# Kernel tuning notes

Measured on AMD Instinct MI355X. Metric: run time of the kernel, lower is better.

## Reference

```python
import jax, jax.numpy as jnp
import numpy as np

# Architecture constants (from module defaults)
D, H, DH, P, G, DEPTH, M, NCLS = 192, 3, 64, 16, 14, 12, 128, 1000  # M = feature_map_dim // 2
EXITS = (4, 8, 12)
TEMP = 1.0 / np.sqrt(DH)  # Favor softmax_temp = 1/sqrt(d_head)
EPS_ATTN = 1e-6           # fast_transformers LinearAttention eps
LN_EPS = 1e-5


def ln(x, g, b):
    mu = x.mean(-1, keepdims=True)
    var = ((x - mu) ** 2).mean(-1, keepdims=True)
    return (x - mu) * jax.lax.rsqrt(var + LN_EPS) * g + b


def favor(x, omega):
    # FAVOR+ positive random features for the softmax kernel.
    # x: [B,L,H,DH], omega: [DH,M] -> phi: [B,L,H,2M]
    xs = x * np.float32(np.sqrt(TEMP))
    off = 0.5 * (xs * xs).sum(-1, keepdims=True)
    u = jnp.einsum('blhd,dm->blhm', xs, omega)
    phi = jnp.concatenate([jnp.exp(u - off), jnp.exp(-u - off)], axis=-1)
    return phi * np.float32(1.0 / np.sqrt(2 * M))


def forward(x, patch_w, patch_b, pe_ln_g, pe_ln_b, cls_token, pos_embed,
            Wq, bq, Wk, bk, Wv, bv, Wo, bo,
            ln1_g, ln1_b, ln2_g, ln2_b, lnb_g, lnb_b,
            W1, b1, W2, b2, omega, head_w, head_b):
    B = x.shape[0]
    # Patch embedding: Conv2d(k=16, s=16) == blocked einsum
    xp = x.reshape(B, 3, G, P, G, P)
    tok = jnp.einsum('bchpwq,dcpq->bhwd', xp, patch_w).reshape(B, G * G, D) + patch_b
    tok = ln(tok, pe_ln_g, pe_ln_b)  # PatchEmbed.norm (norm_layer=LayerNorm)
    tok = jnp.concatenate([jnp.broadcast_to(cls_token, (B, 1, D)), tok], axis=1) + pos_embed
    xc = tok  # [B, 197, D]
    outs = []
    for i in range(DEPTH):
        # --- linear (FAVOR) attention ---
        q = (xc @ Wq[i].T + bq[i]).reshape(B, -1, H, DH)
        k = (xc @ Wk[i].T + bk[i]).reshape(B, -1, H, DH)
        v = (xc @ Wv[i].T + bv[i]).reshape(B, -1, H, DH)
        Qp = favor(q, omega[i])
        Kp = favor(k, omega[i])
        KV = jnp.einsum('bshm,bshd->bhmd', Kp, v)
        Z = 1.0 / (jnp.einsum('blhm,bhm->blh', Qp, Kp.sum(axis=1)) + EPS_ATTN)
        attn = jnp.einsum('blhm,bhmd,blh->blhd', Qp, KV, Z).reshape(B, -1, D)
        # fast_transformers TransformerEncoderLayer (post-norm style)
        xc = xc + attn @ Wo[i].T + bo[i]
        y = xc = ln(xc, ln1_g[i], ln1_b[i])
        y = jax.nn.relu(y @ W1[i].T + b1[i]) @ W2[i].T + b2[i]
        xc = ln(xc + y, ln2_g[i], ln2_b[i])
        # per-block TransformerEncoder final norm (builder final_normalization)
        xc = ln(xc, lnb_g[i], lnb_b[i])
        if (i + 1) in EXITS:
            j = EXITS.index(i + 1)
            z = xc.mean(axis=1)  # AdaptiveAvgPool1d(1) over sequence
            outs.append(z @ head_w[j].T + head_b[j])
    return tuple(outs)


def setup_inputs() -> dict:
    key = jax.random.key(0)
    ks = iter(jax.random.split(key, 32))
    n = lambda shape, s=0.02: jax.random.normal(next(ks), shape, jnp.float32) * s
    return dict(
        x=jax.random.normal(next(ks), (64, 3, 224, 224), jnp.float32),
        patch_w=n((D, 3, P, P)), patch_b=jnp.zeros((D,), jnp.float32),
        pe_ln_g=jnp.ones((D,), jnp.float32), pe_ln_b=jnp.zeros((D,), jnp.float32),
        cls_token=n((1, 1, D)), pos_embed=n((1, G * G + 1, D)),
        Wq=n((DEPTH, D, D)), bq=jnp.zeros((DEPTH, D), jnp.float32),
        Wk=n((DEPTH, D, D)), bk=jnp.zeros((DEPTH, D), jnp.float32),
        Wv=n((DEPTH, D, D)), bv=jnp.zeros((DEPTH, D), jnp.float32),
        Wo=n((DEPTH, D, D)), bo=jnp.zeros((DEPTH, D), jnp.float32),
        ln1_g=jnp.ones((DEPTH, D), jnp.float32), ln1_b=jnp.zeros((DEPTH, D), jnp.float32),
        ln2_g=jnp.ones((DEPTH, D), jnp.float32), ln2_b=jnp.zeros((DEPTH, D), jnp.float32),
        lnb_g=jnp.ones((DEPTH, D), jnp.float32), lnb_b=jnp.zeros((DEPTH, D), jnp.float32),
        W1=n((DEPTH, 4 * D, D)), b1=jnp.zeros((DEPTH, 4 * D), jnp.float32),
        W2=n((DEPTH, D, 4 * D)), b2=jnp.zeros((DEPTH, D), jnp.float32),
        omega=jax.random.normal(next(ks), (DEPTH, DH, M), jnp.float32),
        head_w=n((len(EXITS), NCLS, D)), head_b=jnp.zeros((len(EXITS), NCLS), jnp.float32),
    )


def reference(x, patch_w, patch_b, pe_ln_g, pe_ln_b, cls_token, pos_embed,
              Wq, bq, Wk, bk, Wv, bv, Wo, bo,
              ln1_g, ln1_b, ln2_g, ln2_b, lnb_g, lnb_b,
              W1, b1, W2, b2, omega, head_w, head_b):
    return forward(x, patch_w, patch_b, pe_ln_g, pe_ln_b, cls_token, pos_embed,
                   Wq, bq, Wk, bk, Wv, bv, Wo, bo,
                   ln1_g, ln1_b, ln2_g, ln2_b, lnb_g, lnb_b,
                   W1, b1, W2, b2, omega, head_w, head_b)
```

## Files before the change

### kernel.cpp

```cpp
#include <hip/hip_runtime.h>
#include <math.h>

#define BB     64
#define LLEN   197
#define BLROWS 12608
#define MPAD   12672
#define DMODEL 192
#define NHEAD  3
#define DHEAD  64
#define M2FEAT 256
#define FFDIM  768
#define NDEPTH 12
#define NCLS   1000
#define NPATCH 196
#define BPROWS 12544
#define KPATCH 768
#define PHIRS  264
#define PHTRS  40
#define VLT    208

#define MODE_PLAIN 0
#define MODE_RELU  1
#define MODE_QKV   2

typedef unsigned short ushort;
typedef __attribute__((ext_vector_type(8))) short bf16x8;
typedef __attribute__((ext_vector_type(4))) float floatx4;
typedef __attribute__((ext_vector_type(4))) short short4v;

__device__ __forceinline__ float wave_reduce_sum(float v) {
#pragma unroll
  for (int s = 32; s > 0; s >>= 1) v += __shfl_xor(v, s, 64);
  return v;
}
__device__ __forceinline__ ushort f2bf(float f) {
  unsigned u = __float_as_uint(f);
  return (ushort)((u + 0x7fffu + ((u >> 16) & 1u)) >> 16);
}
__device__ __forceinline__ float bf2f(ushort u) {
  return __uint_as_float(((unsigned)u) << 16);
}
__device__ __forceinline__ void gll16(const ushort* g, ushort* l) {
  __builtin_amdgcn_global_load_lds(
      (const __attribute__((address_space(1))) void*)g,
      (__attribute__((address_space(3))) void*)l, 16, 0, 0);
}

__global__ void zero_buf(uint4* __restrict__ p, int n16) {
  const int i = blockIdx.x * 256 + threadIdx.x;
  if (i < n16) p[i] = uint4{0, 0, 0, 0};
}

__global__ __launch_bounds__(256) void gemm_128(
    const ushort* __restrict__ A, int lda,
    const ushort* __restrict__ W, int ldw,
    const float* __restrict__ bias,
    ushort* __restrict__ C, int ldc, ushort* __restrict__ Vt,
    int Ndim, int Kdim, int mode)
{
  __shared__ __align__(16) ushort As[2][128 * 64];
  __shared__ __align__(16) ushort Ws[2][128 * 64];
  const int tid = threadIdx.x;
  const int bm = blockIdx.x, bn = blockIdx.y;
  const int wave = tid >> 6, lane = tid & 63;
  const int wm = (wave >> 1) * 64, wn = (wave & 1) * 64;
  const int quad = lane >> 4, l16 = lane & 15;
  const int srow = lane >> 3;
  const int scol = ((lane & 7) ^ srow) * 8;
  const ushort* Ap = A + (size_t)(bm * 128) * lda;
  const ushort* Wp = W + (size_t)(bn * 128) * ldw;
  floatx4 acc[4][4] = {};
  const int nT = Kdim >> 6;
#pragma unroll
  for (int t = 0; t < 4; ++t) {
    const int rb = (t * 4 + wave) * 8;
    gll16(Ap + (size_t)(rb + srow) * lda + scol, &As[0][rb * 64]);
    gll16(Wp + (size_t)(rb + srow) * ldw + scol, &Ws[0][rb * 64]);
  }
  for (int kt = 0; kt < nT; ++kt) {
    const int cur = kt & 1;
    __syncthreads();
    if (kt + 1 < nT) {
      const int kk = (kt + 1) * 64, nxt = cur ^ 1;
#pragma unroll
      for (int t = 0; t < 4; ++t) {
        const int rb = (t * 4 + wave) * 8;
        gll16(Ap + (size_t)(rb + srow) * lda + kk + scol, &As[nxt][rb * 64]);
        gll16(Wp + (size_t)(rb + srow) * ldw + kk + scol, &Ws[nxt][rb * 64]);
      }
    }
#pragma unroll
    for (int ks = 0; ks < 2; ++ks) {
      bf16x8 af[4], bf[4];
#pragma unroll
      for (int i = 0; i < 4; ++i) {
        const int ra = wm + i * 16 + l16, rw = wn + i * 16 + l16;
        af[i] = *(const bf16x8*)&As[cur][ra * 64 + ((((ks << 2) | quad) ^ (ra & 7)) * 8)];
        bf[i] = *(const bf16x8*)&Ws[cur][rw * 64 + ((((ks << 2) | quad) ^ (rw & 7)) * 8)];
      }
#pragma unroll
      for (int i = 0; i < 4; ++i)
#pragma unroll
        for (int j = 0; j < 4; ++j)
          acc[i][j] = __builtin_amdgcn_mfma_f32_16x16x32_bf16(af[i], bf[j], acc[i][j], 0, 0, 0);
    }
  }
  if (mode == MODE_QKV) {
#pragma unroll
    for (int i = 0; i < 4; ++i)
#pragma unroll
      for (int r = 0; r < 4; ++r) {
        const int grow = bm * 128 + wm + i * 16 + quad * 4 + r;
        const int bidx = grow / 197;
        const int lloc = grow - bidx * 197;
#pragma unroll
        for (int j = 0; j < 4; ++j) {
          const int col = bn * 128 + wn + j * 16 + l16;
          if (col >= Ndim) continue;
          const float o = acc[i][j][r] + bias[col];
          if (col < 384) {
            C[(size_t)grow * ldc + col] = f2bf(o);
          } else if (grow < BLROWS) {
            const int h = (col - 384) >> 6, d = (col - 384) & 63;
            Vt[((size_t)(bidx * 3 + h) * 64 + d) * VLT + lloc] = f2bf(o);
          }
        }
      }
  } else {
#pragma unroll
    for (int j = 0; j < 4; ++j) {
      const int col = bn * 128 + wn + j * 16 + l16;
      if (col >= Ndim) continue;
      const float bv = bias[col];
#pragma unroll
      for (int i = 0; i < 4; ++i)
#pragma unroll
        for (int r = 0; r < 4; ++r) {
          const int grow = bm * 128 + wm + i * 16 + quad * 4 + r;
          float o = acc[i][j][r] + bv;
          if (mode == MODE_RELU) o = fmaxf(o, 0.f);
          C[(size_t)grow * ldc + col] = f2bf(o);
        }
    }
  }
}

__global__ __launch_bounds__(256) void gemm_bf2(
    const ushort* __restrict__ A, int lda,
    const ushort* __restrict__ W, int ldw,
    const float* __restrict__ bias,
    ushort* __restrict__ C, int ldc, int Kdim, int mode)
{
  __shared__ __align__(16) ushort As[2][128 * 64];
  __shared__ __align__(16) ushort Ws[2][64 * 64];
  const int tid = threadIdx.x;
  const int bm = blockIdx.x, bn = blockIdx.y;
  const int wave = tid >> 6, lane = tid & 63;
  const int wm = (wave >> 1) * 64, wn = (wave & 1) * 32;
  const int quad = lane >> 4, l16 = lane & 15;
  const int srow = lane >> 3;
  const int scol = ((lane & 7) ^ srow) * 8;
  const ushort* Ap = A + (size_t)(bm * 128) * lda;
  const ushort* Wp = W + (size_t)(bn * 64) * ldw;
  floatx4 acc[4][2] = {};
  const int nT = Kdim >> 6;
#pragma unroll
  for (int t = 0; t < 4; ++t) {
    const int rb = (t * 4 + wave) * 8;
    gll16(Ap + (size_t)(rb + srow) * lda + scol, &As[0][rb * 64]);
  }
#pragma unroll
  for (int t = 0; t < 2; ++t) {
    const int rb = (t * 4 + wave) * 8;
    gll16(Wp + (size_t)(rb + srow) * ldw + scol, &Ws[0][rb * 64]);
  }
  for (int kt = 0; kt < nT; ++kt) {
    const int cur = kt & 1;
    __syncthreads();
    if (kt + 1 < nT) {
      const int kk = (kt + 1) * 64, nxt = cur ^ 1;
#pragma unroll
      for (int t = 0; t < 4; ++t) {
        const int rb = (t * 4 + wave) * 8;
        gll16(Ap + (size_t)(rb + srow) * lda + kk + scol, &As[nxt][rb * 64]);
      }
#pragma unroll
      for (int t = 0; t < 2; ++t) {
        const int rb = (t * 4 + wave) * 8;
        gll16(Wp + (size_t)(rb + srow) * ldw + kk + scol, &Ws[nxt][rb * 64]);
      }
    }
#pragma unroll
    for (int ks = 0; ks < 2; ++ks) {
      bf16x8 af[4], bf[2];
#pragma unroll
      for (int i = 0; i < 4; ++i) {
        const int ra = wm + i * 16 + l16;
        af[i] = *(const bf16x8*)&As[cur][ra * 64 + ((((ks << 2) | quad) ^ (ra & 7)) * 8)];
      }
#pragma unroll
      for (int j = 0; j < 2; ++j) {
        const int rw = wn + j * 16 + l16;
        bf[j] = *(const bf16x8*)&Ws[cur][rw * 64 + ((((ks << 2) | quad) ^ (rw & 7)) * 8)];
      }
#pragma unroll
      for (int i = 0; i < 4; ++i)
#pragma unroll
        for (int j = 0; j < 2; ++j)
          acc[i][j] = __builtin_amdgcn_mfma_f32_16x16x32_bf16(af[i], bf[j], acc[i][j], 0, 0, 0);
    }
  }
#pragma unroll
  for (int j = 0; j < 2; ++j) {
    const int col = bn * 64 + wn + j * 16 + l16;
    const float bv = bias[col];
#pragma unroll
    for (int i = 0; i < 4; ++i)
#pragma unroll
      for (int r = 0; r < 4; ++r) {
        const int grow = bm * 128 + wm + i * 16 + quad * 4 + r;
        float o = acc[i][j][r] + bv;
        if (mode == MODE_RELU) o = fmaxf(o, 0.f);
        C[(size_t)grow * ldc + col] = f2bf(o);
      }
  }
}

__global__ __launch_bounds__(256) void gemm_ln(
    const ushort* __restrict__ A, int lda,
    const ushort* __restrict__ W, int ldw,
    const float* __restrict__ bias,
    ushort* __restrict__ XC,
    const float* __restrict__ ga, const float* __restrict__ ba,
    const float* __restrict__ gb, const float* __restrict__ bb,
    int Kdim, int dln)
{
  __shared__ __align__(16) ushort As[2][64 * 64];
  __shared__ __align__(16) ushort Ws[2][192 * 64];
  const int tid = threadIdx.x;
  const int bm = blockIdx.x;
  const int wave = tid >> 6, lane = tid & 63;
  const int quad = lane >> 4, l16 = lane & 15;
  const int srow = lane >> 3;
  const int scol = ((lane & 7) ^ srow) * 8;
  const ushort* Ap = A + (size_t)(bm * 64) * lda;
  floatx4 acc[12] = {};
  const int nT = Kdim >> 6;
#pragma unroll
  for (int t = 0; t < 2; ++t) {
    const int rb = (t * 4 + wave) * 8;
    gll16(Ap + (size_t)(rb + srow) * lda + scol, &As[0][rb * 64]);
  }
#pragma unroll
  for (int t = 0; t < 6; ++t) {
    const int rb = (t * 4 + wave) * 8;
    gll16(W + (size_t)(rb + srow) * ldw + scol, &Ws[0][rb * 64]);
  }
  for (int kt = 0; kt < nT; ++kt) {
    const int cur = kt & 1;
    __syncthreads();
    if (kt + 1 < nT) {
      const int kk = (kt + 1) * 64, nxt = cur ^ 1;
#pragma unroll
      for (int t = 0; t < 2; ++t) {
        const int rb = (t * 4 + wave) * 8;
        gll16(Ap + (size_t)(rb + srow) * lda + kk + scol, &As[nxt][rb * 64]);
      }
#pragma unroll
      for (int t = 0; t < 6; ++t) {
        const int rb = (t * 4 + wave) * 8;
        gll16(W + (size_t)(rb + srow) * ldw + kk + scol, &Ws[nxt][rb * 64]);
      }
    }
#pragma unroll
    for (int ks = 0; ks < 2; ++ks) {
      const int ra = wave * 16 + l16;
      const bf16x8 af = *(const bf16x8*)&As[cur][ra * 64 + ((((ks << 2) | quad) ^ (ra & 7)) * 8)];
#pragma unroll
      for (int j = 0; j < 12; ++j) {
        const int rw = j * 16 + l16;
        const bf16x8 bf = *(const bf16x8*)&Ws[cur][rw * 64 + ((((ks << 2) | quad) ^ (rw & 7)) * 8)];
        acc[j] = __builtin_amdgcn_mfma_f32_16x16x32_bf16(af, bf, acc[j], 0, 0, 0);
      }
    }
  }
#pragma unroll
  for (int r = 0; r < 4; ++r) {
    const int row = bm * 64 + wave * 16 + quad * 4 + r;
    ushort* xp = XC + (size_t)row * DMODEL;
    float xr[12];
    float s = 0.f, sq = 0.f;
#pragma unroll
    for (int j = 0; j < 12; ++j) {
      const int col = j * 16 + l16;
      const float o = acc[j][r] + bias[col] + bf2f(xp[col]);
      xr[j] = o; s += o; sq += o * o;
    }
#pragma unroll
    for (int m = 1; m < 16; m <<= 1) {
      s += __shfl_xor(s, m, 64); sq += __shfl_xor(sq, m, 64);
    }
    float mu = s * (1.f / 192.f);
    float var = sq * (1.f / 192.f) - mu * mu;
    float rs = rsqrtf(var + 1e-5f);
#pragma unroll
    for (int j = 0; j < 12; ++j) {
      const int col = j * 16 + l16;
      xr[j] = (xr[j] - mu) * rs * ga[col] + ba[col];
    }
    if (dln) {
      float s2 = 0.f, sq2 = 0.f;
#pragma unroll
      for (int j = 0; j < 12; ++j) { s2 += xr[j]; sq2 += xr[j] * xr[j]; }
#pragma unroll
      for (int m = 1; m < 16; m <<= 1) {
        s2 += __shfl_xor(s2, m, 64); sq2 += __shfl_xor(sq2, m, 64);
      }
      mu = s2 * (1.f / 192.f);
      var = sq2 * (1.f / 192.f) - mu * mu;
      rs = rsqrtf(var + 1e-5f);
#pragma unroll
      for (int j = 0; j < 12; ++j) {
        const int col = j * 16 + l16;
        xr[j] = (xr[j] - mu) * rs * gb[col] + bb[col];
      }
    }
#pragma unroll
    for (int j = 0; j < 12; ++j) xp[j * 16 + l16] = f2bf(xr[j]);
  }
}

__global__ __launch_bounds__(256) void kv_fused(
    const ushort* __restrict__ qkv, const ushort* __restrict__ OmT,
    const ushort* __restrict__ Vt, ushort* __restrict__ KVt)
{
  __shared__ __align__(16) ushort Ks[32 * 64];
  __shared__ __align__(16) ushort Om[64 * 64];
  __shared__ __align__(16) ushort PhT[128 * PHTRS];
  __shared__ __align__(16) ushort Vts[2][64 * 32];
  __shared__ __align__(16) ushort Vcst[16 * 32];
  __shared__ float offs[32];
  const int tid = threadIdx.x;
  const int bh = blockIdx.x, mh = blockIdx.y;
  const int b = bh / 3, h = bh - b * 3;
  const int wave = tid >> 6, lane = tid & 63;
  const int quad = lane >> 4, l16 = lane & 15;
  const int lr8 = lane >> 3, g8 = lane & 7;
  const int lr4 = lane >> 2, g4 = lane & 3;
#pragma unroll
  for (int t = 0; t < 2; ++t) {
    const int rb = (t * 4 + wave) * 8;
    const int row = rb + lr8;
    gll16(OmT + (size_t)(mh * 64 + row) * 64 + ((g8 ^ (row & 7)) * 8), &Om[rb * 64]);
  }
  {
    const int rowK = wave * 8 + lr8;
    gll16(qkv + (size_t)(b * 197 + rowK) * 576 + 192 + h * 64 + ((g8 ^ (rowK & 7)) * 8),
          &Ks[wave * 8 * 64]);
    const int rowV = wave * 16 + lr4;
    gll16(Vt + ((size_t)bh * 64 + rowV) * VLT + ((g4 ^ (rowV & 3)) * 8),
          &Vts[0][wave * 16 * 32]);
  }
  for (int e = tid; e < 16 * 32; e += 256) Vcst[e] = (e < 32) ? 0x3F80 : 0;
  floatx4 acc[2][5] = {};
  for (int c = 0; c < 7; ++c) {
    const int l0 = c * 32;
    const int cur = c & 1;
    __syncthreads();
    if (tid < 64) {
      const int row = tid >> 1, half = tid & 1;
      float s = 0.f;
#pragma unroll
      for (int t = 0; t < 4; ++t) {
        bf16x8 v8 = *(const bf16x8*)&Ks[row * 64 + (((half * 4 + t) ^ (row & 7)) * 8)];
#pragma unroll
        for (int q = 0; q < 8; ++q) { float xv = bf2f((ushort)v8[q]); s += xv * xv; }
      }
      s += __shfl_xor(s, 1, 64);
      if (half == 0) offs[row] = 0.0625f * s;
    }
    floatx4 ui[2] = {};
#pragma unroll
    for (int ksb = 0; ksb < 2; ++ksb) {
      bf16x8 af[2], bfm;
#pragma unroll
      for (int i = 0; i < 2; ++i) {
        const int row = i * 16 + l16;
        af[i] = *(const bf16x8*)&Ks[row * 64 + (((quad + (ksb << 2)) ^ (row & 7)) * 8)];
      }
      {
        const int row = wave * 16 + l16;
        bfm = *(const bf16x8*)&Om[row * 64 + (((quad + (ksb << 2)) ^ (row & 7)) * 8)];
      }
#pragma unroll
      for (int i = 0; i < 2; ++i)
        ui[i] = __builtin_amdgcn_mfma_f32_16x16x32_bf16(af[i], bfm, ui[i], 0, 0, 0);
    }
    __syncthreads();
    {
      const int mloc = wave * 16 + l16;
#pragma unroll
      for (int i = 0; i < 2; ++i) {
#pragma unroll
        for (int r = 0; r < 4; ++r) {
          const int ll = i * 16 + quad * 4 + r;
          float ep = 0.f, em = 0.f;
          if (l0 + ll < 197) {
            const float off = offs[ll];
            const float u = ui[i][r];
            ep = __expf(u - off) * 0.0625f;
            em = __expf(-u - off) * 0.0625f;
          }
          PhT[mloc * PHTRS + ll] = f2bf(ep);
          PhT[(64 + mloc) * PHTRS + ll] = f2bf(em);
        }
      }
    }
    if (c + 1 < 7) {
      const int rowK = wave * 8 + lr8;
      const int lK = (c + 1) * 32 + rowK;
      gll16(qkv + (size_t)(b * 197 + lK) * 576 + 192 + h * 64 + ((g8 ^ (rowK & 7)) * 8),
            &Ks[wave * 8 * 64]);
      const int rowV = wave * 16 + lr4;
      gll16(Vt + ((size_t)bh * 64 + rowV) * VLT + (c + 1) * 32 + ((g4 ^ (rowV & 3)) * 8),
            &Vts[cur ^ 1][wave * 16 * 32]);
    }
    __syncthreads();
    bf16x8 af[2], bf[5];
#pragma unroll
    for (int i = 0; i < 2; ++i)
      af[i] = *(const bf16x8*)&PhT[(wave * 32 + i * 16 + l16) * PHTRS + quad * 8];
#pragma unroll
    for (int j = 0; j < 4; ++j) {
      const int row = j * 16 + l16;
      bf[j] = *(const bf16x8*)&Vts[cur][row * 32 + ((quad ^ (row & 3)) * 8)];
    }
    bf[4] = *(const bf16x8*)&Vcst[l16 * 32 + quad * 8];
#pragma unroll
    for (int i = 0; i < 2; ++i)
#pragma unroll
      for (int j = 0; j < 5; ++j)
        acc[i][j] = __builtin_amdgcn_mfma_f32_16x16x32_bf16(af[i], bf[j], acc[i][j], 0, 0, 0);
  }
#pragma unroll
  for (int i = 0; i < 2; ++i) {
    const int prow0 = wave * 32 + i * 16 + quad * 4;
    const int f0 = (prow0 < 64) ? (mh * 64 + prow0) : (128 + mh * 64 + prow0 - 64);
#pragma unroll
    for (int j = 0; j < 5; ++j) {
      const int d = j * 16 + l16;
      short4v pk;
#pragma unroll
      for (int r = 0; r < 4; ++r) pk[r] = (short)f2bf(acc[i][j][r]);
      *(short4v*)(KVt + ((size_t)bh * 80 + d) * 256 + f0) = pk;
    }
  }
}

__global__ __launch_bounds__(256) void attn_fused(
    const ushort* __restrict__ qkv, const ushort* __restrict__ OmT,
    const ushort* __restrict__ KVt, ushort* __restrict__ OUT)
{
  __shared__ __align__(16) ushort Phi[64 * PHIRS];
  __shared__ __align__(16) ushort Bs[2][80 * 32];
  __shared__ float offs[64];
  __shared__ float zs[64];
  ushort* Qs = Phi;
  ushort* Om = Phi + 64 * 64;
  const int tid = threadIdx.x;
  const int bx = blockIdx.x, bh = blockIdx.y;
  const int b = bh / 3, h = bh - b * 3;
  const int wave = tid >> 6, lane = tid & 63;
  const int quad = lane >> 4, l16 = lane & 15;
  const int lr8 = lane >> 3, g8 = lane & 7;
  const int lr4 = lane >> 2, g4 = lane & 3;
#pragma unroll
  for (int t = 0; t < 2; ++t) {
    const int rb = wave * 16 + t * 8;
    const int row = rb + lr8;
    const int l = bx * 64 + row;
    gll16(qkv + (size_t)(b * 197 + l) * 576 + h * 64 + ((g8 ^ (row & 7)) * 8), &Qs[rb * 64]);
  }
#pragma unroll
  for (int t = 0; t < 4; ++t) {
    const int rb = wave * 32 + t * 8;
    const int row = rb + lr8;
    gll16(OmT + (size_t)row * 64 + ((g8 ^ (row & 7)) * 8), &Om[rb * 64]);
  }
  __syncthreads();
  if (tid < 128) {
    const int row = tid >> 1, half = tid & 1;
    float s = 0.f;
#pragma unroll
    for (int t = 0; t < 4; ++t) {
      bf16x8 v8 = *(const bf16x8*)&Qs[row * 64 + (((half * 4 + t) ^ (row & 7)) * 8)];
#pragma unroll
      for (int q = 0; q < 8; ++q) { float xv = bf2f((ushort)v8[q]); s += xv * xv; }
    }
    s += __shfl_xor(s, 1, 64);
    if (half == 0) offs[row] = 0.0625f * s;
  }
  floatx4 uacc[8] = {};
#pragma unroll
  for (int ksb = 0; ksb < 2; ++ksb) {
    bf16x8 af, bf[8];
    {
      const int row = wave * 16 + l16;
      af = *(const bf16x8*)&Qs[row * 64 + (((quad + (ksb << 2)) ^ (row & 7)) * 8)];
    }
#pragma unroll
    for (int j = 0; j < 8; ++j) {
      const int row = j * 16 + l16;
      bf[j] = *(const bf16x8*)&Om[row * 64 + (((quad + (ksb << 2)) ^ (row & 7)) * 8)];
    }
#pragma unroll
    for (int j = 0; j < 8; ++j)
      uacc[j] = __builtin_amdgcn_mfma_f32_16x16x32_bf16(af, bf[j], uacc[j], 0, 0, 0);
  }
  __syncthreads();
#pragma unroll
  for (int r = 0; r < 4; ++r) {
    const int l = wave * 16 + quad * 4 + r;
    const float off = offs[l];
#pragma unroll
    for (int j = 0; j < 8; ++j) {
      const int m = j * 16 + l16;
      const float u = uacc[j][r];
      Phi[l * PHIRS + m]       = f2bf(__expf(u - off)  * 0.0625f);
      Phi[l * PHIRS + m + 128] = f2bf(__expf(-u - off) * 0.0625f);
    }
  }
  const ushort* Bp = KVt + (size_t)bh * 80 * 256;
  {
    const int row = wave * 16 + lr4;
    gll16(Bp + (size_t)row * 256 + ((g4 ^ (row & 3)) * 8), &Bs[0][wave * 16 * 32]);
    if (wave == 0)
      gll16(Bp + (size_t)(64 + lr4) * 256 + ((g4 ^ (lr4 & 3)) * 8), &Bs[0][64 * 32]);
  }
  floatx4 acc[5] = {};
  for (int c = 0; c < 8; ++c) {
    const int cur = c & 1;
    __syncthreads();
    if (c + 1 < 8) {
      const int m0 = (c + 1) * 32, nxt = cur ^ 1;
      const int row = wave * 16 + lr4;
      gll16(Bp + (size_t)row * 256 + m0 + ((g4 ^ (row & 3)) * 8), &Bs[nxt][wave * 16 * 32]);
      if (wave == 0)
        gll16(Bp + (size_t)(64 + lr4) * 256 + m0 + ((g4 ^ (lr4 & 3)) * 8), &Bs[nxt][64 * 32]);
    }
    const int m0 = c * 32;
    bf16x8 af, bf[5];
    af = *(const bf16x8*)&Phi[(wave * 16 + l16) * PHIRS + m0 + quad * 8];
#pragma unroll
    for (int j = 0; j < 5; ++j) {
      const int row = j * 16 + l16;
      bf[j] = *(const bf16x8*)&Bs[cur][row * 32 + ((quad ^ (row & 3)) * 8)];
    }
#pragma unroll
    for (int j = 0; j < 5; ++j)
      acc[j] = __builtin_amdgcn_mfma_f32_16x16x32_bf16(af, bf[j], acc[j], 0, 0, 0);
  }
  if (l16 == 0) {
#pragma unroll
    for (int r = 0; r < 4; ++r)
      zs[wave * 16 + quad * 4 + r] = acc[4][r];
  }
  __syncthreads();
#pragma unroll
  for (int r = 0; r < 4; ++r) {
    const int ll = wave * 16 + quad * 4 + r;
    const int l = bx * 64 + ll;
    if (l >= 197) continue;
    const float z = 1.f / (zs[ll] + 1e-6f);
#pragma unroll
    for (int j = 0; j < 4; ++j)
      OUT[(size_t)(b * 197 + l) * 192 + h * 64 + j * 16 + l16] =
          f2bf(acc[j][r] * z);
  }
}

__global__ void conv_qkv(const float* __restrict__ Wq, const float* __restrict__ Wk,
                         const float* __restrict__ Wv, const float* __restrict__ bq,
                         const float* __restrict__ bk, const float* __restrict__ bv,
                         ushort* __restrict__ dst, float* __restrict__ bdst) {
  const int l = blockIdx.y;
  const int e = blockIdx.x * 256 + threadIdx.x;
  const int n = e / 192, k = e - n * 192;
  const float* src;
  if (n < 192)      src = Wq + (size_t)l * 36864 + n * 192;
  else if (n < 384) src = Wk + (size_t)l * 36864 + (n - 192) * 192;
  else              src = Wv + (size_t)l * 36864 + (n - 384) * 192;
  dst[(size_t)l * 640 * 192 + e] = f2bf(src[k]);
  if (e < 576) {
    float bvv;
    if (e < 192)      bvv = bq[l * 192 + e];
    else if (e < 384) bvv = bk[l * 192 + e - 192];
    else              bvv = bv[l * 192 + e - 384];
    bdst[l * 576 + e] = bvv;
  }
}

__global__ void conv_pad(const float* __restrict__ src, ushort* __restrict__ dst,
                         int NK, int padNK) {
  const int l = blockIdx.y;
  const int e = blockIdx.x * 256 + threadIdx.x;
  if (e < NK) dst[(size_t)l * padNK + e] = f2bf(src[(size_t)l * NK + e]);
}

__global__ void conv_omt(const float* __restrict__ om, ushort* __restrict__ dst) {
  const int l = blockIdx.y;
  const int e = blockIdx.x * 256 + threadIdx.x;
  const int m = e >> 6, d = e & 63;
  dst[(size_t)l * 8192 + e] = f2bf(0.35355339059327379f * om[(size_t)l * 8192 + d * 128 + m]);
}

__global__ __launch_bounds__(256) void im2col_kernel(
    const float* __restrict__ X, ushort* __restrict__ Apd)
{
  const int bp = blockIdx.x;
  const int b = bp / NPATCH, p = bp - b * NPATCH;
  const int gh = p / 14, gw = p - gh * 14;
  for (int e = threadIdx.x; e < KPATCH; e += 256) {
    const int c = e >> 8, rem = e & 255, ph = rem >> 4, pw = rem & 15;
    Apd[(size_t)bp * KPATCH + e] =
        f2bf(X[((size_t)(b * 3 + c) * 224 + gh * 16 + ph) * 224 + gw * 16 + pw]);
  }
}

__global__ __launch_bounds__(256) void assemble_kernel(
    const ushort* __restrict__ TK, const float* __restrict__ g,
    const float* __restrict__ bt, const float* __restrict__ cls,
    const float* __restrict__ pos, ushort* __restrict__ XC)
{
  const int w = threadIdx.x >> 6, lane = threadIdx.x & 63;
  const int row = blockIdx.x * 4 + w;
  const int b = row / LLEN, l = row - b * LLEN;
  float o0, o1, o2;
  if (l == 0) {
    o0 = cls[lane]; o1 = cls[lane + 64]; o2 = cls[lane + 128];
  } else {
    const ushort* tp = TK + (size_t)(b * NPATCH + l - 1) * DMODEL;
    const float x0 = bf2f(tp[lane]), x1 = bf2f(tp[lane + 64]), x2 = bf2f(tp[lane + 128]);
    const float s  = wave_reduce_sum(x0 + x1 + x2);
    const float sq = wave_reduce_sum(x0 * x0 + x1 * x1 + x2 * x2);
    const float mu = s * (1.f / 192.f);
    const float var = sq * (1.f / 192.f) - mu * mu;
    const float rs = rsqrtf(var + 1e-5f);
    o0 = (x0 - mu) * rs * g[lane]       + bt[lane];
    o1 = (x1 - mu) * rs * g[lane + 64]  + bt[lane + 64];
    o2 = (x2 - mu) * rs * g[lane + 128] + bt[lane + 128];
  }
  o0 += pos[l * DMODEL + lane];
  o1 += pos[l * DMODEL + lane + 64];
  o2 += pos[l * DMODEL + lane + 128];
  ushort* xp = XC + (size_t)row * DMODEL;
  xp[lane] = f2bf(o0); xp[lane + 64] = f2bf(o1); xp[lane + 128] = f2bf(o2);
}

__global__ __launch_bounds__(256) void head_kernel(
    const ushort* __restrict__ XC, const float* __restrict__ HW,
    const float* __restrict__ HB, float* __restrict__ OUTp)
{
  __shared__ float zsh[DMODEL];
  const int b = blockIdx.y;
  const int tid = threadIdx.x;
  const int wave = tid >> 6, lane = tid & 63;
  if (wave < 3) {
    const int d = wave * 64 + lane;
    const ushort* xp = XC + (size_t)b * LLEN * DMODEL + d;
    float s = 0.f;
#pragma unroll 4
    for (int l = 0; l < LLEN; ++l) s += bf2f(xp[(size_t)l * DMODEL]);
    zsh[d] = s * (1.f / 197.f);
  }
  __syncthreads();
  const int n = blockIdx.x * 256 + tid;
  if (n < NCLS) {
    const float* w = HW + (size_t)n * DMODEL;
    float s = HB[n];
#pragma unroll 4
    for (int d = 0; d < DMODEL; ++d) s = fmaf(zsh[d], w[d], s);
    OUTp[(size_t)b * NCLS + n] = s;
  }
}

extern "C" void kernel_launch(void* const* d_in, const int* in_sizes, int n_in,
                              void* d_out, int out_size, void* d_ws, size_t ws_size,
                              hipStream_t stream) {
  const float* x        = (const float*)d_in[0];
  const float* patch_w  = (const float*)d_in[1];
  const float* patch_b  = (const float*)d_in[2];
  const float* pe_ln_g  = (const float*)d_in[3];
  const float* pe_ln_b  = (const float*)d_in[4];
  const float* cls_tok  = (const float*)d_in[5];
  const float* pos_emb  = (const float*)d_in[6];
  const float* Wq = (const float*)d_in[7];
  const float* bq = (const float*)d_in[8];
  const float* Wk = (const float*)d_in[9];
  const float* bk = (const float*)d_in[10];
  const float* Wv = (const float*)d_in[11];
  const float* bv = (const float*)d_in[12];
  const float* Wo = (const float*)d_in[13];
  const float* bo = (const float*)d_in[14];
  const float* ln1_g = (const float*)d_in[15];
  const float* ln1_b = (const float*)d_in[16];
  const float* ln2_g = (const float*)d_in[17];
  const float* ln2_b = (const float*)d_in[18];
  const float* lnb_g = (const float*)d_in[19];
  const float* lnb_b = (const float*)d_in[20];
  const float* W1 = (const float*)d_in[21];
  const float* b1 = (const float*)d_in[22];
  const float* W2 = (const float*)d_in[23];
  const float* b2 = (const float*)d_in[24];
  const float* omega  = (const float*)d_in[25];
  const float* head_w = (const float*)d_in[26];
  const float* head_b = (const float*)d_in[27];
  float* out = (float*)d_out;
  char* wsb = (char*)d_ws;

  size_t off = 0;
  auto carve = [&](size_t bytes) { size_t o = off; off += (bytes + 255) & ~(size_t)255; return o; };
  ushort* xc     = (ushort*)(wsb + carve((size_t)MPAD * 192 * 2));
  ushort* qkv    = (ushort*)(wsb + carve((size_t)MPAD * 576 * 2));
  ushort* ab     = (ushort*)(wsb + carve((size_t)MPAD * 192 * 2));
  ushort* hidden = (ushort*)(wsb + carve((size_t)MPAD * 768 * 2));
  ushort* KVt    = (ushort*)(wsb + carve((size_t)192 * 80 * 256 * 2));
  ushort* Vt     = (ushort*)(wsb + carve((size_t)192 * 64 * VLT * 2 + 1024));
  float*  bqkv   = (float*)(wsb + carve((size_t)12 * 576 * 4));
  ushort* Wqkv_bf = (ushort*)(wsb + carve((size_t)12 * 640 * 192 * 2));
  ushort* Wo_bf   = (ushort*)(wsb + carve((size_t)12 * 256 * 192 * 2));
  ushort* W1_bf   = (ushort*)(wsb + carve((size_t)12 * 768 * 192 * 2));
  ushort* W2_bf   = (ushort*)(wsb + carve((size_t)12 * 256 * 768 * 2));
  ushort* Wp_bf   = (ushort*)(wsb + carve((size_t)256 * 768 * 2));
  ushort* Om_bf   = (ushort*)(wsb + carve((size_t)12 * 128 * 64 * 2));
  ushort* i2c     = hidden;

  {
    const int n16 = (int)(((size_t)192 * 64 * VLT * 2 + 1024) / 16);
    zero_buf<<<(n16 + 255) / 256, 256, 0, stream>>>((uint4*)Vt, n16);
  }

  conv_qkv<<<dim3(432, 12), 256, 0, stream>>>(Wq, Wk, Wv, bq, bk, bv, Wqkv_bf, bqkv);
  conv_pad<<<dim3(144, 12), 256, 0, stream>>>(Wo, Wo_bf, 36864, 256 * 192);
  conv_pad<<<dim3(576, 12), 256, 0, stream>>>(W1, W1_bf, 147456, 768 * 192);
  conv_pad<<<dim3(576, 12), 256, 0, stream>>>(W2, W2_bf, 147456, 256 * 768);
  conv_pad<<<dim3(576, 1), 256, 0, stream>>>(patch_w, Wp_bf, 147456, 256 * 768);
  conv_omt<<<dim3(32, 12), 256, 0, stream>>>(omega, Om_bf);

  im2col_kernel<<<BPROWS, 256, 0, stream>>>(x, i2c);
  gemm_bf2<<<dim3(98, 3), 256, 0, stream>>>(i2c, KPATCH, Wp_bf, KPATCH,
      patch_b, ab, DMODEL, KPATCH, MODE_PLAIN);
  assemble_kernel<<<BLROWS / 4, 256, 0, stream>>>(ab, pe_ln_g, pe_ln_b,
                                                  cls_tok, pos_emb, xc);

  const int exits[3] = {3, 7, 11};
  for (int i = 0; i < NDEPTH; ++i) {
    gemm_128<<<dim3(99, 5), 256, 0, stream>>>(xc, DMODEL,
        Wqkv_bf + (size_t)i * 640 * 192, DMODEL, bqkv + i * 576,
        qkv, 576, Vt, 576, DMODEL, MODE_QKV);
    kv_fused<<<dim3(192, 2), 256, 0, stream>>>(qkv,
        Om_bf + (size_t)i * 8192, Vt, KVt);
    attn_fused<<<dim3(4, 192), 256, 0, stream>>>(qkv,
        Om_bf + (size_t)i * 8192, KVt, ab);
    gemm_ln<<<MPAD / 64, 256, 0, stream>>>(ab, DMODEL,
        Wo_bf + (size_t)i * 256 * 192, DMODEL, bo + i * DMODEL, xc,
        ln1_g + i * DMODEL, ln1_b + i * DMODEL, nullptr, nullptr,
        DMODEL, 0);
    gemm_128<<<dim3(99, 6), 256, 0, stream>>>(xc, DMODEL,
        W1_bf + (size_t)i * 768 * 192, DMODEL, b1 + i * FFDIM,
        hidden, FFDIM, nullptr, FFDIM, DMODEL, MODE_RELU);
    gemm_ln<<<MPAD / 64, 256, 0, stream>>>(hidden, FFDIM,
        W2_bf + (size_t)i * 256 * 768, FFDIM, b2 + i * DMODEL, xc,
        ln2_g + i * DMODEL, ln2_b + i * DMODEL,
        lnb_g + i * DMODEL, lnb_b + i * DMODEL,
        FFDIM, 1);

    for (int j = 0; j < 3; ++j) {
      if (i == exits[j]) {
        head_kernel<<<dim3(4, BB), 256, 0, stream>>>(
            xc, head_w + (size_t)j * NCLS * DMODEL, head_b + (size_t)j * NCLS,
            out + (size_t)j * BB * NCLS);
      }
    }
  }
}
```

Measured before the change: 1.491 ms.

## Shrink GEMM tiles and split LN-fused GEMM rows across waves

Drops the 128x128 GEMM kernel and routes the QKV and FFN1 projections through the 128x64-tile kernel, which gains the QKV epilogue that scatters V transposed. The LayerNorm-fused output GEMM moves from 64-row to 32-row blocks, with each row's 192 columns split across two waves and row statistics combined through shared memory. The aim is more blocks per launch and better CU fill on these small-N problems. In exchange it reloads more A data, adds barriers and shared-memory reductions, and wastes the padded QKV column tile less.

After: 1.322 ms. -11.3%, faster.

```diff
diff --git a/kernel.cpp b/kernel.cpp
--- a/kernel.cpp
+++ b/kernel.cpp
@@ -51,105 +51,12 @@
   if (i < n16) p[i] = uint4{0, 0, 0, 0};
 }
 
-__global__ __launch_bounds__(256) void gemm_128(
+__global__ __launch_bounds__(256) void gemm_bf2(
     const ushort* __restrict__ A, int lda,
     const ushort* __restrict__ W, int ldw,
     const float* __restrict__ bias,
     ushort* __restrict__ C, int ldc, ushort* __restrict__ Vt,
-    int Ndim, int Kdim, int mode)
-{
-  __shared__ __align__(16) ushort As[2][128 * 64];
-  __shared__ __align__(16) ushort Ws[2][128 * 64];
-  const int tid = threadIdx.x;
-  const int bm = blockIdx.x, bn = blockIdx.y;
-  const int wave = tid >> 6, lane = tid & 63;
-  const int wm = (wave >> 1) * 64, wn = (wave & 1) * 64;
-  const int quad = lane >> 4, l16 = lane & 15;
-  const int srow = lane >> 3;
-  const int scol = ((lane & 7) ^ srow) * 8;
-  const ushort* Ap = A + (size_t)(bm * 128) * lda;
-  const ushort* Wp = W + (size_t)(bn * 128) * ldw;
-  floatx4 acc[4][4] = {};
-  const int nT = Kdim >> 6;
-#pragma unroll
-  for (int t = 0; t < 4; ++t) {
-    const int rb = (t * 4 + wave) * 8;
-    gll16(Ap + (size_t)(rb + srow) * lda + scol, &As[0][rb * 64]);
-    gll16(Wp + (size_t)(rb + srow) * ldw + scol, &Ws[0][rb * 64]);
-  }
-  for (int kt = 0; kt < nT; ++kt) {
-    const int cur = kt & 1;
-    __syncthreads();
-    if (kt + 1 < nT) {
-      const int kk = (kt + 1) * 64, nxt = cur ^ 1;
-#pragma unroll
-      for (int t = 0; t < 4; ++t) {
-        const int rb = (t * 4 + wave) * 8;
-        gll16(Ap + (size_t)(rb + srow) * lda + kk + scol, &As[nxt][rb * 64]);
-        gll16(Wp + (size_t)(rb + srow) * ldw + kk + scol, &Ws[nxt][rb * 64]);
-      }
-    }
-#pragma unroll
-    for (int ks = 0; ks < 2; ++ks) {
-      bf16x8 af[4], bf[4];
-#pragma unroll
-      for (int i = 0; i < 4; ++i) {
-        const int ra = wm + i * 16 + l16, rw = wn + i * 16 + l16;
-        af[i] = *(const bf16x8*)&As[cur][ra * 64 + ((((ks << 2) | quad) ^ (ra & 7)) * 8)];
-        bf[i] = *(const bf16x8*)&Ws[cur][rw * 64 + ((((ks << 2) | quad) ^ (rw & 7)) * 8)];
-      }
-#pragma unroll
-      for (int i = 0; i < 4; ++i)
-#pragma unroll
-        for (int j = 0; j < 4; ++j)
-          acc[i][j] = __builtin_amdgcn_mfma_f32_16x16x32_bf16(af[i], bf[j], acc[i][j], 0, 0, 0);
-    }
-  }
-  if (mode == MODE_QKV) {
-#pragma unroll
-    for (int i = 0; i < 4; ++i)
-#pragma unroll
-      for (int r = 0; r < 4; ++r) {
-        const int grow = bm * 128 + wm + i * 16 + quad * 4 + r;
-        const int bidx = grow / 197;
-        const int lloc = grow - bidx * 197;
-#pragma unroll
-        for (int j = 0; j < 4; ++j) {
-          const int col = bn * 128 + wn + j * 16 + l16;
-          if (col >= Ndim) continue;
-          const float o = acc[i][j][r] + bias[col];
-          if (col < 384) {
-            C[(size_t)grow * ldc + col] = f2bf(o);
-          } else if (grow < BLROWS) {
-            const int h = (col - 384) >> 6, d = (col - 384) & 63;
-            Vt[((size_t)(bidx * 3 + h) * 64 + d) * VLT + lloc] = f2bf(o);
-          }
-        }
-      }
-  } else {
-#pragma unroll
-    for (int j = 0; j < 4; ++j) {
-      const int col = bn * 128 + wn + j * 16 + l16;
-      if (col >= Ndim) continue;
-      const float bv = bias[col];
-#pragma unroll
-      for (int i = 0; i < 4; ++i)
-#pragma unroll
-        for (int r = 0; r < 4; ++r) {
-          const int grow = bm * 128 + wm + i * 16 + quad * 4 + r;
-          float o = acc[i][j][r] + bv;
-          if (mode == MODE_RELU) o = fmaxf(o, 0.f);
-          C[(size_t)grow * ldc + col] = f2bf(o);
-        }
-    }
-  }
-}
-
-__global__ __launch_bounds__(256) void gemm_bf2(
-    const ushort* __restrict__ A, int lda,
-    const ushort* __restrict__ W, int ldw,
-    const float* __restrict__ bias,
-    ushort* __restrict__ C, int ldc, int Kdim, int mode)
+    int Kdim, int mode)
 {
   __shared__ __align__(16) ushort As[2][128 * 64];
   __shared__ __align__(16) ushort Ws[2][64 * 64];
@@ -210,19 +117,41 @@
           acc[i][j] = __builtin_amdgcn_mfma_f32_16x16x32_bf16(af[i], bf[j], acc[i][j], 0, 0, 0);
     }
   }
-#pragma unroll
-  for (int j = 0; j < 2; ++j) {
-    const int col = bn * 64 + wn + j * 16 + l16;
-    const float bv = bias[col];
+  if (mode == MODE_QKV) {
 #pragma unroll
     for (int i = 0; i < 4; ++i)
 #pragma unroll
       for (int r = 0; r < 4; ++r) {
         const int grow = bm * 128 + wm + i * 16 + quad * 4 + r;
-        float o = acc[i][j][r] + bv;
-        if (mode == MODE_RELU) o = fmaxf(o, 0.f);
-        C[(size_t)grow * ldc + col] = f2bf(o);
-      }
+        const int bidx = grow / 197;
+        const int lloc = grow - bidx * 197;
+#pragma unroll
+        for (int j = 0; j < 2; ++j) {
+          const int col = bn * 64 + wn + j * 16 + l16;
+          const float o = acc[i][j][r] + bias[col];
+          if (col < 384) {
+            C[(size_t)grow * ldc + col] = f2bf(o);
+          } else if (grow < BLROWS) {
+            const int h = (col - 384) >> 6, d = (col - 384) & 63;
+            Vt[((size_t)(bidx * 3 + h) * 64 + d) * VLT + lloc] = f2bf(o);
+          }
+        }
+      }
+  } else {
+#pragma unroll
+    for (int j = 0; j < 2; ++j) {
+      const int col = bn * 64 + wn + j * 16 + l16;
+      const float bv = bias[col];
+#pragma unroll
+      for (int i = 0; i < 4; ++i)
+#pragma unroll
+        for (int r = 0; r < 4; ++r) {
+          const int grow = bm * 128 + wm + i * 16 + quad * 4 + r;
+          float o = acc[i][j][r] + bv;
+          if (mode == MODE_RELU) o = fmaxf(o, 0.f);
+          C[(size_t)grow * ldc + col] = f2bf(o);
+        }
+    }
   }
 }
 
@@ -235,22 +164,20 @@
     const float* __restrict__ gb, const float* __restrict__ bb,
     int Kdim, int dln)
 {
-  __shared__ __align__(16) ushort As[2][64 * 64];
+  __shared__ __align__(16) ushort As[2][32 * 64];
   __shared__ __align__(16) ushort Ws[2][192 * 64];
+  __shared__ float p1s[2][32], p1q[2][32], p2s[2][32], p2q[2][32];
   const int tid = threadIdx.x;
   const int bm = blockIdx.x;
   const int wave = tid >> 6, lane = tid & 63;
+  const int rg = wave >> 1, cg = wave & 1;
   const int quad = lane >> 4, l16 = lane & 15;
   const int srow = lane >> 3;
   const int scol = ((lane & 7) ^ srow) * 8;
-  const ushort* Ap = A + (size_t)(bm * 64) * lda;
-  floatx4 acc[12] = {};
+  const ushort* Ap = A + (size_t)(bm * 32) * lda;
+  floatx4 acc[6] = {};
   const int nT = Kdim >> 6;
-#pragma unroll
-  for (int t = 0; t < 2; ++t) {
-    const int rb = (t * 4 + wave) * 8;
-    gll16(Ap + (size_t)(rb + srow) * lda + scol, &As[0][rb * 64]);
-  }
+  gll16(Ap + (size_t)(wave * 8 + srow) * lda + scol, &As[0][wave * 8 * 64]);
 #pragma unroll
   for (int t = 0; t < 6; ++t) {
     const int rb = (t * 4 + wave) * 8;
@@ -261,11 +188,7 @@
     __syncthreads();
     if (kt + 1 < nT) {
       const int kk = (kt + 1) * 64, nxt = cur ^ 1;
-#pragma unroll
-      for (int t = 0; t < 2; ++t) {
-        const int rb = (t * 4 + wave) * 8;
-        gll16(Ap + (size_t)(rb + srow) * lda + kk + scol, &As[nxt][rb * 64]);
-      }
+      gll16(Ap + (size_t)(wave * 8 + srow) * lda + kk + scol, &As[nxt][wave * 8 * 64]);
 #pragma unroll
       for (int t = 0; t < 6; ++t) {
         const int rb = (t * 4 + wave) * 8;
@@ -274,59 +197,85 @@
     }
 #pragma unroll
     for (int ks = 0; ks < 2; ++ks) {
-      const int ra = wave * 16 + l16;
+      const int ra = rg * 16 + l16;
       const bf16x8 af = *(const bf16x8*)&As[cur][ra * 64 + ((((ks << 2) | quad) ^ (ra & 7)) * 8)];
 #pragma unroll
-      for (int j = 0; j < 12; ++j) {
-        const int rw = j * 16 + l16;
+      for (int j = 0; j < 6; ++j) {
+        const int rw = (cg * 6 + j) * 16 + l16;
         const bf16x8 bf = *(const bf16x8*)&Ws[cur][rw * 64 + ((((ks << 2) | quad) ^ (rw & 7)) * 8)];
         acc[j] = __builtin_amdgcn_mfma_f32_16x16x32_bf16(af, bf, acc[j], 0, 0, 0);
       }
     }
   }
+  float xr[4][6];
 #pragma unroll
   for (int r = 0; r < 4; ++r) {
-    const int row = bm * 64 + wave * 16 + quad * 4 + r;
-    ushort* xp = XC + (size_t)row * DMODEL;
-    float xr[12];
+    const int rloc = rg * 16 + quad * 4 + r;
+    const int row = bm * 32 + rloc;
+    const ushort* xp = XC + (size_t)row * DMODEL;
     float s = 0.f, sq = 0.f;
 #pragma unroll
-    for (int j = 0; j < 12; ++j) {
-      const int col = j * 16 + l16;
+    for (int j = 0; j < 6; ++j) {
+      const int col = (cg * 6 + j) * 16 + l16;
       const float o = acc[j][r] + bias[col] + bf2f(xp[col]);
-      xr[j] = o; s += o; sq += o * o;
+      xr[r][j] = o; s += o; sq += o * o;
     }
 #pragma unroll
     for (int m = 1; m < 16; m <<= 1) {
       s += __shfl_xor(s, m, 64); sq += __shfl_xor(sq, m, 64);
     }
-    float mu = s * (1.f / 192.f);
-    float var = sq * (1.f / 192.f) - mu * mu;
-    float rs = rsqrtf(var + 1e-5f);
-#pragma unroll
-    for (int j = 0; j < 12; ++j) {
-      const int col = j * 16 + l16;
-      xr[j] = (xr[j] - mu) * rs * ga[col] + ba[col];
-    }
-    if (dln) {
-      float s2 = 0.f, sq2 = 0.f;
-#pragma unroll
-      for (int j = 0; j < 12; ++j) { s2 += xr[j]; sq2 += xr[j] * xr[j]; }
+    if (l16 == 0) { p1s[cg][rloc] = s; p1q[cg][rloc] = sq; }
+  }
+  __syncthreads();
+#pragma unroll
+  for (int r = 0; r < 4; ++r) {
+    const int rloc = rg * 16 + quad * 4 + r;
+    const float s = p1s[0][rloc] + p1s[1][rloc];
+    const float sq = p1q[0][rloc] + p1q[1][rloc];
+    const float mu = s * (1.f / 192.f);
+    const float var = sq * (1.f / 192.f) - mu * mu;
+    const float rs = rsqrtf(var + 1e-5f);
+#pragma unroll
+    for (int j = 0; j < 6; ++j) {
+      const int col = (cg * 6 + j) * 16 + l16;
+      xr[r][j] = (xr[r][j] - mu) * rs * ga[col] + ba[col];
+    }
+  }
+  if (dln) {
+#pragma unroll
+    for (int r = 0; r < 4; ++r) {
+      const int rloc = rg * 16 + quad * 4 + r;
+      float s = 0.f, sq = 0.f;
+#pragma unroll
+      for (int j = 0; j < 6; ++j) { s += xr[r][j]; sq += xr[r][j] * xr[r][j]; }
 #pragma unroll
       for (int m = 1; m < 16; m <<= 1) {
-        s2 += __shfl_xor(s2, m, 64); sq2 += __shfl_xor(sq2, m, 64);
-      }
-      mu = s2 * (1.f / 192.f);
-      var = sq2 * (1.f / 192.f) - mu * mu;
-      rs = rsqrtf(var + 1e-5f);
-#pragma unroll
-      for (int j = 0; j < 12; ++j) {
-        const int col = j * 16 + l16;
-        xr[j] = (xr[j] - mu) * rs * gb[col] + bb[col];
-      }
-    }
-#pragma unroll
-    for (int j = 0; j < 12; ++j) xp[j * 16 + l16] = f2bf(xr[j]);
+        s += __shfl_xor(s, m, 64); sq += __shfl_xor(sq, m, 64);
+      }
+      if (l16 == 0) { p2s[cg][rloc] = s; p2q[cg][rloc] = sq; }
+    }
+    __syncthreads();
+#pragma unroll
+    for (int r = 0; r < 4; ++r) {
+      const int rloc = rg * 16 + quad * 4 + r;
+      const float s = p2s[0][rloc] + p2s[1][rloc];
+      const float sq = p2q[0][rloc] + p2q[1][rloc];
+      const float mu = s * (1.f / 192.f);
+      const float var = sq * (1.f / 192.f) - mu * mu;
+      const float rs = rsqrtf(var + 1e-5f);
+#pragma unroll
+      for (int j = 0; j < 6; ++j) {
+        const int col = (cg * 6 + j) * 16 + l16;
+        xr[r][j] = (xr[r][j] - mu) * rs * gb[col] + bb[col];
+      }
+    }
+  }
+#pragma unroll
+  for (int r = 0; r < 4; ++r) {
+    const int row = bm * 32 + rg * 16 + quad * 4 + r;
+    ushort* xp = XC + (size_t)row * DMODEL;
+#pragma unroll
+    for (int j = 0; j < 6; ++j) xp[(cg * 6 + j) * 16 + l16] = f2bf(xr[r][j]);
   }
 }
 
@@ -749,27 +698,27 @@
 
   im2col_kernel<<<BPROWS, 256, 0, stream>>>(x, i2c);
   gemm_bf2<<<dim3(98, 3), 256, 0, stream>>>(i2c, KPATCH, Wp_bf, KPATCH,
-      patch_b, ab, DMODEL, KPATCH, MODE_PLAIN);
+      patch_b, ab, DMODEL, nullptr, KPATCH, MODE_PLAIN);
   assemble_kernel<<<BLROWS / 4, 256, 0, stream>>>(ab, pe_ln_g, pe_ln_b,
                                                   cls_tok, pos_emb, xc);
 
   const int exits[3] = {3, 7, 11};
   for (int i = 0; i < NDEPTH; ++i) {
-    gemm_128<<<dim3(99, 5), 256, 0, stream>>>(xc, DMODEL,
+    gemm_bf2<<<dim3(99, 9), 256, 0, stream>>>(xc, DMODEL,
         Wqkv_bf + (size_t)i * 640 * 192, DMODEL, bqkv + i * 576,
-        qkv, 576, Vt, 576, DMODEL, MODE_QKV);
+        qkv, 576, Vt, DMODEL, MODE_QKV);
     kv_fused<<<dim3(192, 2), 256, 0, stream>>>(qkv,
         Om_bf + (size_t)i * 8192, Vt, KVt);
     attn_fused<<<dim3(4, 192), 256, 0, stream>>>(qkv,
         Om_bf + (size_t)i * 8192, KVt, ab);
-    gemm_ln<<<MPAD / 64, 256, 0, stream>>>(ab, DMODEL,
+    gemm_ln<<<MPAD / 32, 256, 0, stream>>>(ab, DMODEL,
         Wo_bf + (size_t)i * 256 * 192, DMODEL, bo + i * DMODEL, xc,
         ln1_g + i * DMODEL, ln1_b + i * DMODEL, nullptr, nullptr,
         DMODEL, 0);
-    gemm_128<<<dim3(99, 6), 256, 0, stream>>>(xc, DMODEL,
+    gemm_bf2<<<dim3(99, 12), 256, 0, stream>>>(xc, DMODEL,
         W1_bf + (size_t)i * 768 * 192, DMODEL, b1 + i * FFDIM,
-        hidden, FFDIM, nullptr, FFDIM, DMODEL, MODE_RELU);
-    gemm_ln<<<MPAD / 64, 256, 0, stream>>>(hidden, FFDIM,
+        hidden, FFDIM, nullptr, DMODEL, MODE_RELU);
+    gemm_ln<<<MPAD / 32, 256, 0, stream>>>(hidden, FFDIM,
         W2_bf + (size_t)i * 256 * 768, FFDIM, b2 + i * DMODEL, xc,
         ln2_g + i * DMODEL, ln2_b + i * DMODEL,
         lnb_g + i * DMODEL, lnb_b + i * DMODEL,
```
